# Kernel optimization log

Hardware: AMD Instinct MI355X
Metric: run time of the kernel (lower is better)

Reference implementation:

```python
import jax, jax.numpy as jnp
import numpy as np

B, D, H, W = 16, 64, 64, 64
K = 1024


def setup_inputs() -> dict:
    key = jax.random.key(0)
    k1, k2 = jax.random.split(key)
    x = jax.random.normal(k1, (B, D, H, W), dtype=jnp.float32)
    limit = 3.0 ** 0.5
    e_i_ts = jax.random.uniform(k2, (D, K), dtype=jnp.float32, minval=-limit, maxval=limit)
    return {"x": x, "e_i_ts": e_i_ts}


def reference(x, e_i_ts):
    b, d, h, w = x.shape
    # [B,H,W,D] -> [N,D]
    flat_x = jnp.transpose(x, (0, 2, 3, 1)).reshape(-1, d)
    distances = (
        jnp.sum(flat_x * flat_x, axis=1, keepdims=True)
        - 2.0 * (flat_x @ e_i_ts)
        + jnp.sum(e_i_ts * e_i_ts, axis=0, keepdims=True)
    )
    encoding_indices = jnp.argmin(distances, axis=1)  # [N]
    reshaped_indices = encoding_indices.reshape(b, h, w)
    # codebook gather: e_i_ts.T is [K,D]
    quantized = jnp.take(e_i_ts.T, reshaped_indices, axis=0)  # [B,H,W,D]
    quantized_x = jnp.transpose(quantized, (0, 3, 1, 2))  # [B,D,H,W]

    dictionary_loss = jnp.mean((jax.lax.stop_gradient(x) - quantized_x) ** 2)
    commitment_loss = jnp.mean((x - jax.lax.stop_gradient(quantized_x)) ** 2)
    # straight-through estimator
    quantized_x = x + jax.lax.stop_gradient(quantized_x - x)
    return quantized_x, dictionary_loss, commitment_loss, encoding_indices.reshape(b, -1)
```

## Files before the change

### kernel.cpp

```cpp
#include <hip/hip_runtime.h>

#define DD 64
#define KK 1024
#define NPTS 65536
#define TOTAL 4194304

#define OFF_L1 4194304
#define OFF_L2 4194305
#define OFF_IDX 4194306

#define WS_ENH_F 64
#define WS_EHT_BYTE 65536
#define WS_ELT_BYTE (65536 + 131072)

#define MARGIN_S 0.006f

typedef __attribute__((ext_vector_type(8))) short short8;
typedef __attribute__((ext_vector_type(4))) float f32x4;

__device__ __forceinline__ unsigned short bf16_rne(float f) {
    unsigned b = __float_as_uint(f);
    return (unsigned short)((b + 0x7FFFu + ((b >> 16) & 1u)) >> 16);
}
__device__ __forceinline__ float bf16_to_f(unsigned short h) {
    return __uint_as_float(((unsigned)h) << 16);
}
__device__ __forceinline__ unsigned umax(unsigned a, unsigned b) { return a > b ? a : b; }
__device__ __forceinline__ unsigned umin(unsigned a, unsigned b) { return a < b ? a : b; }
__device__ __forceinline__ void gld_lds16(const void* g, void* l) {
    __builtin_amdgcn_global_load_lds(
        (const __attribute__((address_space(1))) void*)g,
        (__attribute__((address_space(3))) void*)l, 16, 0, 0);
}
__device__ __forceinline__ int swz(int r, int d) {
    return ((d & ~7) ^ ((r & 7) << 3)) | (d & 7);
}

__global__ __launch_bounds__(256) void prep_kernel(const float* __restrict__ e,
                                                   float* __restrict__ enh,
                                                   unsigned short* __restrict__ ehT,
                                                   unsigned short* __restrict__ elT,
                                                   float* __restrict__ sum,
                                                   unsigned* __restrict__ tick) {
    const int tid = threadIdx.x;
    if (blockIdx.x == 0 && tid == 0) { *sum = 0.f; *tick = 0u; }
    const int wave = tid >> 6, lane = tid & 63;
    const int k = blockIdx.x * 4 + wave;
    const float v = e[lane * KK + k];
    const unsigned short h = bf16_rne(v);
    const unsigned short l = bf16_rne(v - bf16_to_f(h));
    const int pos = k * 64 + swz(k, lane);
    ehT[pos] = h;
    elT[pos] = l;
    float s2 = v * v;
#pragma unroll
    for (int m = 32; m > 0; m >>= 1) s2 += __shfl_down(s2, m, 64);
    if (lane == 0) enh[k] = 512.0f - 0.5f * s2;
}

__global__ __launch_bounds__(256, 4) void vq_gemm(const float* __restrict__ x,
                                                  const float* __restrict__ e,
                                                  const float* __restrict__ enh,
                                                  const unsigned short* __restrict__ ehT,
                                                  const unsigned short* __restrict__ elT,
                                                  float* __restrict__ out,
                                                  float* __restrict__ sum,
                                                  unsigned* __restrict__ tick) {
    __shared__ __align__(16) char ebuf[2 * 16384];

    float* mv1 = (float*)ebuf;
    float* mv2 = mv1 + 128;
    int*   mi1 = (int*)(mv2 + 128);
    int*   ks  = mi1 + 128;
    float* xnp = (float*)(ks + 64);
    float* lv  = xnp + 64;
    float* xp  = lv + 64;
    int*   rl  = (int*)(xp + 64);
    int*   rn  = rl + 64;
    float* rv  = (float*)(rn + 1);
    int*   ri  = (int*)(rv + 4);

    const int tid = threadIdx.x;
    const int wave = tid >> 6, lane = tid & 63;
    const int n0 = blockIdx.x * 64;
    const int b = n0 >> 12;
    const int hw0 = n0 & 4095;

    const char* ehTb = (const char*)ehT;
    const char* elTb = (const char*)elT;
    const int lofs = wave * 1024 + lane * 16;

    {
        char* db = ebuf;
        gld_lds16(ehTb + lofs,        db + wave * 1024);
        gld_lds16(ehTb + 4096 + lofs, db + 4096 + wave * 1024);
        gld_lds16(elTb + lofs,        db + 8192 + wave * 1024);
        gld_lds16(elTb + 4096 + lofs, db + 12288 + wave * 1024);
    }

    float* xsc = (float*)(ebuf + 16384);
    {
        const int d = tid >> 2, ph = tid & 3;
        const float* src = x + ((b * DD + d) << 12) + hw0 + ph * 16;
        float* dst = xsc + d * 64 + ph * 16;
#pragma unroll
        for (int j = 0; j < 4; ++j)
            *(float4*)(dst + j * 4) = *(const float4*)(src + j * 4);
    }
    __syncthreads();
    const int p = tid >> 2, dq = tid & 3;
    float xv[16];
    float xn = 0.f;
#pragma unroll
    for (int s = 0; s < 16; ++s) {
        xv[s] = xsc[(dq * 16 + s) * 64 + p];
        xn = fmaf(xv[s], xv[s], xn);
    }
    xn += __shfl_down(xn, 1, 64);
    xn += __shfl_down(xn, 2, 64);
    __syncthreads();
    unsigned short* xbh = (unsigned short*)(ebuf + 16384);
    unsigned short* xbl = (unsigned short*)(ebuf + 16384 + 8192);
    {
#pragma unroll
        for (int g = 0; g < 2; ++g) {
            short8 hh, ll;
#pragma unroll
            for (int j = 0; j < 8; ++j) {
                const float f = xv[g * 8 + j];
                const unsigned short h = bf16_rne(f);
                hh[j] = (short)h;
                ll[j] = (short)bf16_rne(f - bf16_to_f(h));
            }
            const int pos = p * 64 + ((dq * 16 + g * 8) ^ ((p & 7) << 3));
            *(short8*)(xbh + pos) = hh;
            *(short8*)(xbl + pos) = ll;
        }
    }
    __syncthreads();

    const int ln15 = lane & 15, q8 = (lane >> 4) * 8;
    const int wp = (wave >> 1) * 32;
    const int wc = (wave & 1) * 32;

    short8 ah[2][2], al[2][2];
#pragma unroll
    for (int rf = 0; rf < 2; ++rf)
#pragma unroll
        for (int kc = 0; kc < 2; ++kc) {
            const int pp = wp + rf * 16 + ln15;
            const int pos = pp * 64 + ((kc * 32 + q8) ^ ((pp & 7) << 3));
            ah[rf][kc] = *(const short8*)(xbh + pos);
            al[rf][kc] = *(const short8*)(xbl + pos);
        }

    unsigned v1u[8], v2u[8];
#pragma unroll
    for (int r = 0; r < 8; ++r) { v1u[r] = 0u; v2u[r] = 0u; }

    for (int kt = 0; kt < 16; ++kt) {
        __syncthreads();
        if (kt < 15) {
            const int nkt = kt + 1;
            char* db = ebuf + (nkt & 1) * 16384;
            const char* sH = ehTb + nkt * 8192 + lofs;
            const char* sL = elTb + nkt * 8192 + lofs;
            gld_lds16(sH,        db + wave * 1024);
            gld_lds16(sH + 4096, db + 4096 + wave * 1024);
            gld_lds16(sL,        db + 8192 + wave * 1024);
            gld_lds16(sL + 4096, db + 12288 + wave * 1024);
        }
        const unsigned short* ebH = (const unsigned short*)(ebuf + (kt & 1) * 16384);
        const unsigned short* ebL = ebH + 4096;

        f32x4 acc[2][2];
#pragma unroll
        for (int cf = 0; cf < 2; ++cf) {
            const float ec = enh[kt * 64 + wc + cf * 16 + ln15];
#pragma unroll
            for (int rf = 0; rf < 2; ++rf)
                acc[rf][cf] = (f32x4){ec, ec, ec, ec};
        }

#pragma unroll
        for (int kc = 0; kc < 2; ++kc) {
            short8 bh[2], bl[2];
#pragma unroll
            for (int cf = 0; cf < 2; ++cf) {
                const int c = wc + cf * 16 + ln15;
                const int pos = c * 64 + ((kc * 32 + q8) ^ ((c & 7) << 3));
                bh[cf] = *(const short8*)(ebH + pos);
                bl[cf] = *(const short8*)(ebL + pos);
            }
#pragma unroll
            for (int rf = 0; rf < 2; ++rf)
#pragma unroll
                for (int cf = 0; cf < 2; ++cf) {
                    acc[rf][cf] = __builtin_amdgcn_mfma_f32_16x16x32_bf16(al[rf][kc], bh[cf], acc[rf][cf], 0, 0, 0);
                    acc[rf][cf] = __builtin_amdgcn_mfma_f32_16x16x32_bf16(ah[rf][kc], bl[cf], acc[rf][cf], 0, 0, 0);
                    acc[rf][cf] = __builtin_amdgcn_mfma_f32_16x16x32_bf16(ah[rf][kc], bh[cf], acc[rf][cf], 0, 0, 0);
                }
        }

#pragma unroll
        for (int rf = 0; rf < 2; ++rf)
#pragma unroll
            for (int reg = 0; reg < 4; ++reg) {
                const int r = rf * 4 + reg;
                const unsigned k0 = (__float_as_uint(acc[rf][0][reg]) | 31u) ^ (unsigned)(kt * 2 + 0);
                const unsigned k1 = (__float_as_uint(acc[rf][1][reg]) | 31u) ^ (unsigned)(kt * 2 + 1);
                const unsigned a = umax(k0, k1), bb = umin(k0, k1);
                v2u[r] = umax(umax(v2u[r], umin(v1u[r], a)), bb);
                v1u[r] = umax(v1u[r], a);
            }
    }

    if ((tid & 3) == 0) xnp[p] = xn;
    if (tid == 0) *rn = 0;

#pragma unroll
    for (int r = 0; r < 8; ++r) {
        const unsigned c5 = 31u - (v1u[r] & 31u);
        int col = (int)(c5 >> 1) * 64 + wc + (int)(c5 & 1) * 16 + ln15;
        float val = __uint_as_float(v1u[r] & ~31u);
        float sec = __uint_as_float(v2u[r] & ~31u);
#pragma unroll
        for (int msk = 1; msk < 16; msk <<= 1) {
            const float ov = __shfl_xor(val, msk);
            const int oc = __shfl_xor(col, msk);
            const float os = __shfl_xor(sec, msk);
            sec = fmaxf(fmaxf(sec, os), fminf(val, ov));
            const bool t = (ov > val) || (ov == val && oc < col);
            val = t ? ov : val;
            col = t ? oc : col;
        }
        if (ln15 == 0) {
            const int q = lane >> 4;
            const int h = wave & 1;
            const int pt = wp + (r >> 2) * 16 + q * 4 + (r & 3);
            mv1[pt * 2 + h] = val;
            mi1[pt * 2 + h] = col;
            mv2[pt * 2 + h] = sec;
        }
    }
    __syncthreads();
    if (tid < 64) {
        const float va = mv1[tid * 2], vb = mv1[tid * 2 + 1];
        const int ia = mi1[tid * 2], ib = mi1[tid * 2 + 1];
        const bool t = (vb > va) || (vb == va && ib < ia);
        const float bv = t ? vb : va;
        const int bi = t ? ib : ia;
        const float sec = fmaxf(fmaxf(mv2[tid * 2], mv2[tid * 2 + 1]), fminf(va, vb));
        ks[tid] = bi;
        const float bmid = __uint_as_float(__float_as_uint(bv) | 16u);
        lv[tid] = xnp[tid] + 1024.0f - 2.0f * bmid;
        if (bv - sec < MARGIN_S) {
            const int w = atomicAdd(rn, 1);
            rl[w] = tid;
        }
    }
    __syncthreads();

    const int lcnt = *rn;
    for (int it = 0; it < lcnt; ++it) {
        const int pr = rl[it];
        if (tid < 64) xp[tid] = x[((b * DD + tid) << 12) + hw0 + pr];
        __syncthreads();
        float d0 = 0.f, d1 = 0.f, d2 = 0.f, d3 = 0.f;
#pragma unroll 8
        for (int dd = 0; dd < DD; ++dd) {
            const float xd = xp[dd];
            const float4 ev = *(const float4*)(e + dd * KK + tid * 4);
            d0 = fmaf(xd, ev.x, d0);
            d1 = fmaf(xd, ev.y, d1);
            d2 = fmaf(xd, ev.z, d2);
            d3 = fmaf(xd, ev.w, d3);
        }
        const float4 ea = *(const float4*)(enh + tid * 4);
        float bs = d0 + ea.x;
        int bi2 = tid * 4;
        if (d1 + ea.y > bs) { bs = d1 + ea.y; bi2 = tid * 4 + 1; }
        if (d2 + ea.z > bs) { bs = d2 + ea.z; bi2 = tid * 4 + 2; }
        if (d3 + ea.w > bs) { bs = d3 + ea.w; bi2 = tid * 4 + 3; }
#pragma unroll
        for (int m = 1; m < 64; m <<= 1) {
            const float ov = __shfl_xor(bs, m, 64);
            const int oi = __shfl_xor(bi2, m, 64);
            if (ov > bs || (ov == bs && oi < bi2)) { bs = ov; bi2 = oi; }
        }
        if (lane == 0) { rv[wave] = bs; ri[wave] = bi2; }
        __syncthreads();
        if (tid == 0) {
            float gs = rv[0];
            int gi = ri[0];
#pragma unroll
            for (int t2 = 1; t2 < 4; ++t2)
                if (rv[t2] > gs || (rv[t2] == gs && ri[t2] < gi)) { gs = rv[t2]; gi = ri[t2]; }
            ks[pr] = gi;
            lv[pr] = xnp[pr] + 1024.0f - 2.0f * gs;
        }
        __syncthreads();
    }

    if (tid < 64) {
        out[OFF_IDX + n0 + tid] = (float)ks[tid];
        float lc = lv[tid];
#pragma unroll
        for (int off = 32; off > 0; off >>= 1) lc += __shfl_down(lc, off, 64);
        if (tid == 0) {
            atomicAdd(sum, lc);
            __threadfence();
            const unsigned old = atomicAdd(tick, 1u);
            if (old == (unsigned)(gridDim.x - 1)) {
                const float s = atomicAdd(sum, 0.0f);
                const float m = s * (1.0f / (float)TOTAL);
                out[OFF_L1] = m;
                out[OFF_L2] = m;
            }
        }
    }

    {
        const int pe = tid & 63, dqr = tid >> 6;
        const int kp = ks[pe];
        const int kx = (kp & 7) << 3;
        float qa[16];
#pragma unroll
        for (int g = 0; g < 2; ++g) {
            const int pos = kp * 64 + ((dqr * 16 + g * 8) ^ kx);
            const short8 h8 = *(const short8*)(ehT + pos);
            const short8 l8 = *(const short8*)(elT + pos);
#pragma unroll
            for (int j = 0; j < 8; ++j)
                qa[g * 8 + j] = bf16_to_f((unsigned short)h8[j]) + bf16_to_f((unsigned short)l8[j]);
        }
        float* ob = out + ((b * DD + dqr * 16) << 12) + hw0 + pe;
#pragma unroll
        for (int s = 0; s < 16; ++s) ob[s << 12] = qa[s];
    }
}

extern "C" void kernel_launch(void* const* d_in, const int* in_sizes, int n_in,
                              void* d_out, int out_size, void* d_ws, size_t ws_size,
                              hipStream_t stream) {
    const float* x = (const float*)d_in[0];
    const float* e = (const float*)d_in[1];
    float* out = (float*)d_out;

    float* sum = (float*)d_ws;
    unsigned* tick = (unsigned*)d_ws + 2;
    float* enh = (float*)d_ws + WS_ENH_F;
    unsigned short* ehT = (unsigned short*)((char*)d_ws + WS_EHT_BYTE);
    unsigned short* elT = (unsigned short*)((char*)d_ws + WS_ELT_BYTE);

    prep_kernel<<<256, 256, 0, stream>>>(e, enh, ehT, elT, sum, tick);
    vq_gemm<<<NPTS / 64, 256, 0, stream>>>(x, e, enh, ehT, elT, out, sum, tick);
}
```

Measured before the change: 136.7 us.

## Triple-buffer codebook tiles with vmcnt waits and load x directly from global

Codebook tile prefetch moves from double to triple buffering with a prefetch distance of two. Each iteration now uses an explicit s_waitcnt vmcnt plus s_barrier in place of a full __syncthreads, so the next load stays in flight during compute. The x tile is read straight from global into registers, dropping the LDS fp32 staging and one barrier, and per-wave partial norms are summed later. The enh bias vector is cached in LDS. LDS use grows to about 53KB and the launch-bounds occupancy hint is removed, which may lower the number of resident blocks.

Result: slower. 146.9 us (+7.5%).

```diff
diff --git a/kernel.cpp b/kernel.cpp
--- a/kernel.cpp
+++ b/kernel.cpp
@@ -58,22 +58,23 @@
     if (lane == 0) enh[k] = 512.0f - 0.5f * s2;
 }
 
-__global__ __launch_bounds__(256, 4) void vq_gemm(const float* __restrict__ x,
-                                                  const float* __restrict__ e,
-                                                  const float* __restrict__ enh,
-                                                  const unsigned short* __restrict__ ehT,
-                                                  const unsigned short* __restrict__ elT,
-                                                  float* __restrict__ out,
-                                                  float* __restrict__ sum,
-                                                  unsigned* __restrict__ tick) {
-    __shared__ __align__(16) char ebuf[2 * 16384];
+__global__ __launch_bounds__(256) void vq_gemm(const float* __restrict__ x,
+                                               const float* __restrict__ e,
+                                               const float* __restrict__ enh,
+                                               const unsigned short* __restrict__ ehT,
+                                               const unsigned short* __restrict__ elT,
+                                               float* __restrict__ out,
+                                               float* __restrict__ sum,
+                                               unsigned* __restrict__ tick) {
+    __shared__ __align__(16) char ebuf[3 * 16384];
+    __shared__ float enh_lds[1024];
+    __shared__ float xnp4[256];
 
     float* mv1 = (float*)ebuf;
     float* mv2 = mv1 + 128;
     int*   mi1 = (int*)(mv2 + 128);
     int*   ks  = mi1 + 128;
-    float* xnp = (float*)(ks + 64);
-    float* lv  = xnp + 64;
+    float* lv  = (float*)(ks + 64);
     float* xp  = lv + 64;
     int*   rl  = (int*)(xp + 64);
     int*   rn  = rl + 64;
@@ -90,38 +91,31 @@
     const char* elTb = (const char*)elT;
     const int lofs = wave * 1024 + lane * 16;
 
+#pragma unroll
+    for (int t0 = 0; t0 < 2; ++t0) {
+        char* db = ebuf + t0 * 16384;
+        const char* sH = ehTb + t0 * 8192 + lofs;
+        const char* sL = elTb + t0 * 8192 + lofs;
+        gld_lds16(sH,        db + wave * 1024);
+        gld_lds16(sH + 4096, db + 4096 + wave * 1024);
+        gld_lds16(sL,        db + 8192 + wave * 1024);
+        gld_lds16(sL + 4096, db + 12288 + wave * 1024);
+    }
+
+    *(float4*)(enh_lds + tid * 4) = *(const float4*)(enh + tid * 4);
+
+    unsigned short* xbh = (unsigned short*)(ebuf + 32768);
+    unsigned short* xbl = xbh + 4096;
     {
-        char* db = ebuf;
-        gld_lds16(ehTb + lofs,        db + wave * 1024);
-        gld_lds16(ehTb + 4096 + lofs, db + 4096 + wave * 1024);
-        gld_lds16(elTb + lofs,        db + 8192 + wave * 1024);
-        gld_lds16(elTb + 4096 + lofs, db + 12288 + wave * 1024);
-    }
-
-    float* xsc = (float*)(ebuf + 16384);
-    {
-        const int d = tid >> 2, ph = tid & 3;
-        const float* src = x + ((b * DD + d) << 12) + hw0 + ph * 16;
-        float* dst = xsc + d * 64 + ph * 16;
-#pragma unroll
-        for (int j = 0; j < 4; ++j)
-            *(float4*)(dst + j * 4) = *(const float4*)(src + j * 4);
-    }
-    __syncthreads();
-    const int p = tid >> 2, dq = tid & 3;
-    float xv[16];
-    float xn = 0.f;
-#pragma unroll
-    for (int s = 0; s < 16; ++s) {
-        xv[s] = xsc[(dq * 16 + s) * 64 + p];
-        xn = fmaf(xv[s], xv[s], xn);
-    }
-    xn += __shfl_down(xn, 1, 64);
-    xn += __shfl_down(xn, 2, 64);
-    __syncthreads();
-    unsigned short* xbh = (unsigned short*)(ebuf + 16384);
-    unsigned short* xbl = (unsigned short*)(ebuf + 16384 + 8192);
-    {
+        const float* xs = x + ((b * DD + wave * 16) << 12) + hw0 + lane;
+        float xv[16];
+        float xn = 0.f;
+#pragma unroll
+        for (int s = 0; s < 16; ++s) {
+            xv[s] = xs[s << 12];
+            xn = fmaf(xv[s], xv[s], xn);
+        }
+        xnp4[tid] = xn;
 #pragma unroll
         for (int g = 0; g < 2; ++g) {
             short8 hh, ll;
@@ -132,7 +126,7 @@
                 hh[j] = (short)h;
                 ll[j] = (short)bf16_rne(f - bf16_to_f(h));
             }
-            const int pos = p * 64 + ((dq * 16 + g * 8) ^ ((p & 7) << 3));
+            const int pos = lane * 64 + ((wave * 16 + g * 8) ^ ((lane & 7) << 3));
             *(short8*)(xbh + pos) = hh;
             *(short8*)(xbl + pos) = ll;
         }
@@ -153,16 +147,20 @@
             ah[rf][kc] = *(const short8*)(xbh + pos);
             al[rf][kc] = *(const short8*)(xbl + pos);
         }
+    __syncthreads();
 
     unsigned v1u[8], v2u[8];
 #pragma unroll
     for (int r = 0; r < 8; ++r) { v1u[r] = 0u; v2u[r] = 0u; }
 
     for (int kt = 0; kt < 16; ++kt) {
-        __syncthreads();
-        if (kt < 15) {
-            const int nkt = kt + 1;
-            char* db = ebuf + (nkt & 1) * 16384;
+        if (kt < 15) asm volatile("s_waitcnt vmcnt(4)" ::: "memory");
+        else         asm volatile("s_waitcnt vmcnt(0)" ::: "memory");
+        asm volatile("s_barrier" ::: "memory");
+        __builtin_amdgcn_sched_barrier(0);
+        if (kt < 14) {
+            const int nkt = kt + 2;
+            char* db = ebuf + (nkt % 3) * 16384;
             const char* sH = ehTb + nkt * 8192 + lofs;
             const char* sL = elTb + nkt * 8192 + lofs;
             gld_lds16(sH,        db + wave * 1024);
@@ -170,13 +168,13 @@
             gld_lds16(sL,        db + 8192 + wave * 1024);
             gld_lds16(sL + 4096, db + 12288 + wave * 1024);
         }
-        const unsigned short* ebH = (const unsigned short*)(ebuf + (kt & 1) * 16384);
+        const unsigned short* ebH = (const unsigned short*)(ebuf + (kt % 3) * 16384);
         const unsigned short* ebL = ebH + 4096;
 
         f32x4 acc[2][2];
 #pragma unroll
         for (int cf = 0; cf < 2; ++cf) {
-            const float ec = enh[kt * 64 + wc + cf * 16 + ln15];
+            const float ec = enh_lds[kt * 64 + wc + cf * 16 + ln15];
 #pragma unroll
             for (int rf = 0; rf < 2; ++rf)
                 acc[rf][cf] = (f32x4){ec, ec, ec, ec};
@@ -215,7 +213,7 @@
             }
     }
 
-    if ((tid & 3) == 0) xnp[p] = xn;
+    __syncthreads();
     if (tid == 0) *rn = 0;
 
 #pragma unroll
@@ -252,8 +250,9 @@
         const int bi = t ? ib : ia;
         const float sec = fmaxf(fmaxf(mv2[tid * 2], mv2[tid * 2 + 1]), fminf(va, vb));
         ks[tid] = bi;
+        const float xnp = xnp4[tid] + xnp4[64 + tid] + xnp4[128 + tid] + xnp4[192 + tid];
         const float bmid = __uint_as_float(__float_as_uint(bv) | 16u);
-        lv[tid] = xnp[tid] + 1024.0f - 2.0f * bmid;
+        lv[tid] = xnp + 1024.0f - 2.0f * bmid;
         if (bv - sec < MARGIN_S) {
             const int w = atomicAdd(rn, 1);
             rl[w] = tid;
@@ -297,7 +296,8 @@
             for (int t2 = 1; t2 < 4; ++t2)
                 if (rv[t2] > gs || (rv[t2] == gs && ri[t2] < gi)) { gs = rv[t2]; gi = ri[t2]; }
             ks[pr] = gi;
-            lv[pr] = xnp[pr] + 1024.0f - 2.0f * gs;
+            const float xnp = xnp4[pr] + xnp4[64 + pr] + xnp4[128 + pr] + xnp4[192 + pr];
+            lv[pr] = xnp + 1024.0f - 2.0f * gs;
         }
         __syncthreads();
     }
```
